# Kernel tuning notes

Hardware: AMD Instinct MI355X
Metric: run time of the kernel (lower is better)

Reference implementation:

```python
import jax, jax.numpy as jnp
import numpy as np

N_NODES = 50000
N_EDGES = 1600000
D_EDGE = 32
D_NODE = 32
D_HID = 128
D_OUT = 32


def setup_inputs() -> dict:
    key = jax.random.key(0)
    ks = jax.random.split(key, 8)
    edge_feats = jax.random.normal(ks[0], (N_EDGES, D_EDGE), dtype=jnp.float32)
    node_feats = jax.random.normal(ks[1], (N_NODES, D_NODE), dtype=jnp.float32)
    senders = jax.random.randint(ks[2], (N_EDGES,), 0, N_NODES, dtype=jnp.int64 if jax.config.jax_enable_x64 else jnp.int32)
    receivers = jax.random.randint(ks[3], (N_EDGES,), 0, N_NODES, dtype=jnp.int64 if jax.config.jax_enable_x64 else jnp.int32)
    d_in = D_EDGE + 2 * D_NODE  # 96
    W1 = jax.random.normal(ks[4], (d_in, D_HID), dtype=jnp.float32) / jnp.sqrt(jnp.float32(d_in))
    b1 = jnp.zeros((D_HID,), dtype=jnp.float32)
    W2 = jax.random.normal(ks[5], (D_HID, D_OUT), dtype=jnp.float32) / jnp.sqrt(jnp.float32(D_HID))
    b2 = jnp.zeros((D_OUT,), dtype=jnp.float32)
    return {"edge_feats": edge_feats, "node_feats": node_feats, "senders": senders,
            "receivers": receivers, "W1": W1, "b1": b1, "W2": W2, "b2": b2}


def reference(edge_feats, node_feats, senders, receivers, W1, b1, W2, b2):
    # Gather node feats to edges (target=0 -> senders, target=1 -> receivers),
    # concat with edge feats along feature dim, then edge MLP.
    sender_feats = node_feats[senders]        # [E, D_NODE]
    receiver_feats = node_feats[receivers]    # [E, D_NODE]
    collected = jnp.concatenate([edge_feats, sender_feats, receiver_feats], axis=1)  # [E, 96]
    h = jax.nn.relu(collected @ W1 + b1)      # [E, 128]
    updated_edges = h @ W2 + b2               # [E, 32]
    return updated_edges
```

## Files before the change

kernel.cpp:

```cpp
#include <hip/hip_runtime.h>

typedef __attribute__((ext_vector_type(8))) short bf16x8;
typedef __attribute__((ext_vector_type(4))) float f32x4;
typedef unsigned short ushort_t;
typedef unsigned int uint32;

#define TILE 64
#define N_EDGES 1600000
#define NT (N_EDGES / TILE)

#define CSTR 104
#define HSTR 136
#define COL_OFF 0
#define H_OFF 0
#define W1_OFF (TILE * HSTR)
#define W2_OFF (W1_OFF + 128 * CSTR)
#define SMEM_USHORTS (W2_OFF + 32 * HSTR)

__device__ __forceinline__ ushort_t f2bf(float x) {
    uint32 u = __builtin_bit_cast(uint32, x);
    u += 0x7FFFu + ((u >> 16) & 1u);
    return (ushort_t)(u >> 16);
}
__device__ __forceinline__ uint32 pack2(float a, float b) {
    return (uint32)f2bf(a) | ((uint32)f2bf(b) << 16);
}
__device__ __forceinline__ void store_bf16x8(ushort_t* dst, f32x4 a, f32x4 b) {
    uint4 p;
    p.x = pack2(a[0], a[1]);
    p.y = pack2(a[2], a[3]);
    p.z = pack2(b[0], b[1]);
    p.w = pack2(b[2], b[3]);
    *reinterpret_cast<uint4*>(dst) = p;
}

__global__ __launch_bounds__(256, 3)
void edge_mlp_kernel(const float* __restrict__ edge_feats,
                     const float* __restrict__ node_feats,
                     const int* __restrict__ senders,
                     const int* __restrict__ receivers,
                     const float* __restrict__ W1,
                     const float* __restrict__ b1,
                     const float* __restrict__ W2,
                     const float* __restrict__ b2,
                     float* __restrict__ out)
{
    __shared__ __align__(16) ushort_t smem[SMEM_USHORTS];
    ushort_t* colbuf = smem + COL_OFF;
    ushort_t* hbuf   = smem + H_OFF;
    ushort_t* w1t    = smem + W1_OFF;
    ushort_t* w2t    = smem + W2_OFF;

    const int tid = threadIdx.x;
    const int l   = tid & 63;
    const int llo = l & 15;
    const int lhi = l >> 4;
    const int w   = tid >> 6;

    for (int idx = tid; idx < 96 * 128; idx += 256) {
        int k = idx >> 7, n = idx & 127;
        w1t[n * CSTR + k] = f2bf(W1[idx]);
    }
    for (int idx = tid; idx < 128 * 32; idx += 256) {
        int n = idx >> 5, o = idx & 31;
        w2t[o * HSTR + n] = f2bf(W2[idx]);
    }

    f32x4 b1v[8], b2v[2];
#pragma unroll
    for (int ni = 0; ni < 8; ++ni)
        b1v[ni] = *reinterpret_cast<const f32x4*>(b1 + ni * 16 + lhi * 4);
#pragma unroll
    for (int oi = 0; oi < 2; ++oi)
        b2v[oi] = *reinterpret_cast<const f32x4*>(b2 + oi * 16 + lhi * 4);

    const int row = tid >> 2;
    const int q   = tid & 3;

    for (int t = blockIdx.x; t < NT; t += gridDim.x) {
        const long e0 = (long)t * TILE;
        const long e  = e0 + row;

        const int si = senders[e];
        const int ri = receivers[e];
        const f32x4* efp = reinterpret_cast<const f32x4*>(edge_feats + e * 32) + q * 2;
        f32x4 ea = efp[0], eb = efp[1];
        const f32x4* sp = reinterpret_cast<const f32x4*>(node_feats + (long)si * 32) + q * 2;
        f32x4 sa = sp[0], sb = sp[1];
        const f32x4* rp = reinterpret_cast<const f32x4*>(node_feats + (long)ri * 32) + q * 2;
        f32x4 ra = rp[0], rb = rp[1];

        __syncthreads();

        store_bf16x8(colbuf + row * CSTR +      q * 8, ea, eb);
        store_bf16x8(colbuf + row * CSTR + 32 + q * 8, sa, sb);
        store_bf16x8(colbuf + row * CSTR + 64 + q * 8, ra, rb);

        __syncthreads();

        f32x4 acc1[8];
#pragma unroll
        for (int ni = 0; ni < 8; ++ni) acc1[ni] = f32x4{0.f, 0.f, 0.f, 0.f};
        const ushort_t* crow = colbuf + (w * 16 + llo) * CSTR + lhi * 8;
        const ushort_t* w1r  = w1t + llo * CSTR + lhi * 8;
#pragma unroll
        for (int kk = 0; kk < 3; ++kk) {
            bf16x8 bfrag = *reinterpret_cast<const bf16x8*>(crow + kk * 32);
#pragma unroll
            for (int ni = 0; ni < 8; ++ni) {
                bf16x8 afrag = *reinterpret_cast<const bf16x8*>(w1r + ni * 16 * CSTR + kk * 32);
                acc1[ni] = __builtin_amdgcn_mfma_f32_16x16x32_bf16(afrag, bfrag, acc1[ni], 0, 0, 0);
            }
        }

        __syncthreads();

#pragma unroll
        for (int ni = 0; ni < 8; ++ni) {
            float h0 = fmaxf(acc1[ni][0] + b1v[ni][0], 0.f);
            float h1 = fmaxf(acc1[ni][1] + b1v[ni][1], 0.f);
            float h2 = fmaxf(acc1[ni][2] + b1v[ni][2], 0.f);
            float h3 = fmaxf(acc1[ni][3] + b1v[ni][3], 0.f);
            uint2 p;
            p.x = pack2(h0, h1);
            p.y = pack2(h2, h3);
            *reinterpret_cast<uint2*>(hbuf + (w * 16 + llo) * HSTR + ni * 16 + lhi * 4) = p;
        }

        __syncthreads();

        f32x4 acc2[2];
        acc2[0] = f32x4{0.f, 0.f, 0.f, 0.f};
        acc2[1] = f32x4{0.f, 0.f, 0.f, 0.f};
        const ushort_t* hrow = hbuf + (w * 16 + llo) * HSTR + lhi * 8;
        const ushort_t* w2r  = w2t + llo * HSTR + lhi * 8;
#pragma unroll
        for (int kk = 0; kk < 4; ++kk) {
            bf16x8 bfrag = *reinterpret_cast<const bf16x8*>(hrow + kk * 32);
#pragma unroll
            for (int oi = 0; oi < 2; ++oi) {
                bf16x8 afrag = *reinterpret_cast<const bf16x8*>(w2r + oi * 16 * HSTR + kk * 32);
                acc2[oi] = __builtin_amdgcn_mfma_f32_16x16x32_bf16(afrag, bfrag, acc2[oi], 0, 0, 0);
            }
        }

        float* orow = out + (e0 + w * 16 + llo) * 32 + lhi * 4;
#pragma unroll
        for (int oi = 0; oi < 2; ++oi) {
            f32x4 r;
            r[0] = acc2[oi][0] + b2v[oi][0];
            r[1] = acc2[oi][1] + b2v[oi][1];
            r[2] = acc2[oi][2] + b2v[oi][2];
            r[3] = acc2[oi][3] + b2v[oi][3];
            *reinterpret_cast<f32x4*>(orow + oi * 16) = r;
        }
    }
}

extern "C" void kernel_launch(void* const* d_in, const int* in_sizes, int n_in,
                              void* d_out, int out_size, void* d_ws, size_t ws_size,
                              hipStream_t stream) {
    const float* edge_feats = (const float*)d_in[0];
    const float* node_feats = (const float*)d_in[1];
    const int*   senders    = (const int*)d_in[2];
    const int*   receivers  = (const int*)d_in[3];
    const float* W1         = (const float*)d_in[4];
    const float* b1         = (const float*)d_in[5];
    const float* W2         = (const float*)d_in[6];
    const float* b2         = (const float*)d_in[7];
    float* out = (float*)d_out;

    dim3 grid(2048), block(256);
    hipLaunchKernelGGL(edge_mlp_kernel, grid, block, 0, stream,
                       edge_feats, node_feats, senders, receivers, W1, b1, W2, b2, out);
}
```

Before: 421.2 us.

## Per-wave private tiles with register prefetch, drop block barriers, shrink grid

Each wave now owns a private 16-row LDS region, so the block-wide __syncthreads inside the tile loop are removed. Gathered features for the next tile and indices for the tile after that are prefetched into registers, overlapping global and gather latency with MFMA work. MFMA sections are wrapped in s_setprio and the grid drops from 2048 to 768 persistent blocks. This raises register pressure and relies on intra-wave ordering for LDS reuse, which is not explicitly guarded.

```diff
diff --git a/kernel.cpp b/kernel.cpp
--- a/kernel.cpp
+++ b/kernel.cpp
@@ -8,12 +8,12 @@
 #define TILE 64
 #define N_EDGES 1600000
 #define NT (N_EDGES / TILE)
+#define GRID 768
 
 #define CSTR 104
 #define HSTR 136
-#define COL_OFF 0
-#define H_OFF 0
-#define W1_OFF (TILE * HSTR)
+#define WBUF (16 * HSTR)
+#define W1_OFF (4 * WBUF)
 #define W2_OFF (W1_OFF + 128 * CSTR)
 #define SMEM_USHORTS (W2_OFF + 32 * HSTR)
 
@@ -46,16 +46,18 @@
                      float* __restrict__ out)
 {
     __shared__ __align__(16) ushort_t smem[SMEM_USHORTS];
-    ushort_t* colbuf = smem + COL_OFF;
-    ushort_t* hbuf   = smem + H_OFF;
-    ushort_t* w1t    = smem + W1_OFF;
-    ushort_t* w2t    = smem + W2_OFF;
+    ushort_t* w1t = smem + W1_OFF;
+    ushort_t* w2t = smem + W2_OFF;
 
     const int tid = threadIdx.x;
     const int l   = tid & 63;
     const int llo = l & 15;
     const int lhi = l >> 4;
     const int w   = tid >> 6;
+    const int r   = l >> 2;
+    const int q   = l & 3;
+
+    ushort_t* buf = smem + w * WBUF;
 
     for (int idx = tid; idx < 96 * 128; idx += 256) {
         int k = idx >> 7, n = idx & 127;
@@ -74,35 +76,54 @@
     for (int oi = 0; oi < 2; ++oi)
         b2v[oi] = *reinterpret_cast<const f32x4*>(b2 + oi * 16 + lhi * 4);
 
-    const int row = tid >> 2;
-    const int q   = tid & 3;
+    __syncthreads();
 
-    for (int t = blockIdx.x; t < NT; t += gridDim.x) {
-        const long e0 = (long)t * TILE;
-        const long e  = e0 + row;
+    const long stride = gridDim.x;
+    const long last = (long)NT - 1;
+    long t = blockIdx.x;
 
-        const int si = senders[e];
-        const int ri = receivers[e];
-        const f32x4* efp = reinterpret_cast<const f32x4*>(edge_feats + e * 32) + q * 2;
-        f32x4 ea = efp[0], eb = efp[1];
-        const f32x4* sp = reinterpret_cast<const f32x4*>(node_feats + (long)si * 32) + q * 2;
-        f32x4 sa = sp[0], sb = sp[1];
-        const f32x4* rp = reinterpret_cast<const f32x4*>(node_feats + (long)ri * 32) + q * 2;
-        f32x4 ra = rp[0], rb = rp[1];
+    long eS = t * TILE + w * 16 + r;
+    int si_c = senders[eS], ri_c = receivers[eS];
+    f32x4 ea, eb, sa, sb, ra, rb;
+    {
+        const f32x4* efp = reinterpret_cast<const f32x4*>(edge_feats + eS * 32) + q * 2;
+        ea = efp[0]; eb = efp[1];
+        const f32x4* sp = reinterpret_cast<const f32x4*>(node_feats + (long)si_c * 32) + q * 2;
+        sa = sp[0]; sb = sp[1];
+        const f32x4* rp = reinterpret_cast<const f32x4*>(node_feats + (long)ri_c * 32) + q * 2;
+        ra = rp[0]; rb = rp[1];
+    }
+    long ts1 = t + stride; ts1 = ts1 <= last ? ts1 : last;
+    long eS1 = ts1 * TILE + w * 16 + r;
+    int si_n = senders[eS1], ri_n = receivers[eS1];
 
-        __syncthreads();
+    for (; t < NT; t += stride) {
+        ushort_t* cw = buf + r * CSTR + q * 8;
+        store_bf16x8(cw,      ea, eb);
+        store_bf16x8(cw + 32, sa, sb);
+        store_bf16x8(cw + 64, ra, rb);
 
-        store_bf16x8(colbuf + row * CSTR +      q * 8, ea, eb);
-        store_bf16x8(colbuf + row * CSTR + 32 + q * 8, sa, sb);
-        store_bf16x8(colbuf + row * CSTR + 64 + q * 8, ra, rb);
-
-        __syncthreads();
+        long tn = t + stride; tn = tn <= last ? tn : last;
+        f32x4 nea, neb, nsa, nsb, nra, nrb;
+        {
+            long eN = tn * TILE + w * 16 + r;
+            const f32x4* efp = reinterpret_cast<const f32x4*>(edge_feats + eN * 32) + q * 2;
+            nea = efp[0]; neb = efp[1];
+            const f32x4* sp = reinterpret_cast<const f32x4*>(node_feats + (long)si_n * 32) + q * 2;
+            nsa = sp[0]; nsb = sp[1];
+            const f32x4* rp = reinterpret_cast<const f32x4*>(node_feats + (long)ri_n * 32) + q * 2;
+            nra = rp[0]; nrb = rp[1];
+        }
+        long tn2 = t + 2 * stride; tn2 = tn2 <= last ? tn2 : last;
+        long eN2 = tn2 * TILE + w * 16 + r;
+        int si_2 = senders[eN2], ri_2 = receivers[eN2];
 
         f32x4 acc1[8];
 #pragma unroll
         for (int ni = 0; ni < 8; ++ni) acc1[ni] = f32x4{0.f, 0.f, 0.f, 0.f};
-        const ushort_t* crow = colbuf + (w * 16 + llo) * CSTR + lhi * 8;
+        const ushort_t* crow = buf + llo * CSTR + lhi * 8;
         const ushort_t* w1r  = w1t + llo * CSTR + lhi * 8;
+        __builtin_amdgcn_s_setprio(1);
 #pragma unroll
         for (int kk = 0; kk < 3; ++kk) {
             bf16x8 bfrag = *reinterpret_cast<const bf16x8*>(crow + kk * 32);
@@ -112,8 +133,7 @@
                 acc1[ni] = __builtin_amdgcn_mfma_f32_16x16x32_bf16(afrag, bfrag, acc1[ni], 0, 0, 0);
             }
         }
-
-        __syncthreads();
+        __builtin_amdgcn_s_setprio(0);
 
 #pragma unroll
         for (int ni = 0; ni < 8; ++ni) {
@@ -124,16 +144,15 @@
             uint2 p;
             p.x = pack2(h0, h1);
             p.y = pack2(h2, h3);
-            *reinterpret_cast<uint2*>(hbuf + (w * 16 + llo) * HSTR + ni * 16 + lhi * 4) = p;
+            *reinterpret_cast<uint2*>(buf + llo * HSTR + ni * 16 + lhi * 4) = p;
         }
-
-        __syncthreads();
 
         f32x4 acc2[2];
         acc2[0] = f32x4{0.f, 0.f, 0.f, 0.f};
         acc2[1] = f32x4{0.f, 0.f, 0.f, 0.f};
-        const ushort_t* hrow = hbuf + (w * 16 + llo) * HSTR + lhi * 8;
+        const ushort_t* hrow = buf + llo * HSTR + lhi * 8;
         const ushort_t* w2r  = w2t + llo * HSTR + lhi * 8;
+        __builtin_amdgcn_s_setprio(1);
 #pragma unroll
         for (int kk = 0; kk < 4; ++kk) {
             bf16x8 bfrag = *reinterpret_cast<const bf16x8*>(hrow + kk * 32);
@@ -143,17 +162,21 @@
                 acc2[oi] = __builtin_amdgcn_mfma_f32_16x16x32_bf16(afrag, bfrag, acc2[oi], 0, 0, 0);
             }
         }
+        __builtin_amdgcn_s_setprio(0);
 
-        float* orow = out + (e0 + w * 16 + llo) * 32 + lhi * 4;
+        float* orow = out + (t * TILE + w * 16 + llo) * 32 + lhi * 4;
 #pragma unroll
         for (int oi = 0; oi < 2; ++oi) {
-            f32x4 r;
-            r[0] = acc2[oi][0] + b2v[oi][0];
-            r[1] = acc2[oi][1] + b2v[oi][1];
-            r[2] = acc2[oi][2] + b2v[oi][2];
-            r[3] = acc2[oi][3] + b2v[oi][3];
-            *reinterpret_cast<f32x4*>(orow + oi * 16) = r;
+            f32x4 rr;
+            rr[0] = acc2[oi][0] + b2v[oi][0];
+            rr[1] = acc2[oi][1] + b2v[oi][1];
+            rr[2] = acc2[oi][2] + b2v[oi][2];
+            rr[3] = acc2[oi][3] + b2v[oi][3];
+            *reinterpret_cast<f32x4*>(orow + oi * 16) = rr;
         }
+
+        ea = nea; eb = neb; sa = nsa; sb = nsb; ra = nra; rb = nrb;
+        si_n = si_2; ri_n = ri_2;
     }
 }
 
@@ -170,7 +193,7 @@
     const float* b2         = (const float*)d_in[7];
     float* out = (float*)d_out;
 
-    dim3 grid(2048), block(256);
+    dim3 grid(GRID), block(256);
     hipLaunchKernelGGL(edge_mlp_kernel, grid, block, 0, stream,
                        edge_feats, node_feats, senders, receivers, W1, b1, W2, b2, out);
 }
```

Result: faster. 388.4 us (-7.8%).
